# Optimization experiments

Measured on AMD Instinct MI355X. Metric: run time of the kernel, lower is better.

Reference implementation:

```python
import jax, jax.numpy as jnp
import numpy as np

D_MODEL = 1024
N_HEADS = 16
SEQ = 512  # == max_seq_len; rel-pos bias requires n_token == max_seq_len


def setup_inputs() -> dict:
    key = jax.random.key(0)
    ks = jax.random.split(key, 12)
    B = 16
    x = jax.random.normal(ks[0], (B, SEQ, D_MODEL), dtype=jnp.float32)
    c = jax.random.normal(ks[1], (B, SEQ, 8), dtype=jnp.float32)  # unused by forward
    s = 1.0 / np.sqrt(D_MODEL)
    Wq = jax.random.normal(ks[2], (D_MODEL, D_MODEL), dtype=jnp.float32) * s
    bq = jnp.zeros((D_MODEL,), dtype=jnp.float32)
    Wk = jax.random.normal(ks[3], (D_MODEL, D_MODEL), dtype=jnp.float32) * s
    bk = jnp.zeros((D_MODEL,), dtype=jnp.float32)
    Wv = jax.random.normal(ks[4], (D_MODEL, D_MODEL), dtype=jnp.float32) * s
    bv = jnp.zeros((D_MODEL,), dtype=jnp.float32)
    Wo = jax.random.normal(ks[5], (D_MODEL, D_MODEL), dtype=jnp.float32) * s
    bo = jnp.zeros((D_MODEL,), dtype=jnp.float32)
    # trunc_normal_(std=0.02) approximated by normal*0.02 (values stay small)
    rel_table = jax.random.normal(ks[6], (2 * SEQ - 1, N_HEADS), dtype=jnp.float32) * 0.02
    return {"x": x, "c": c, "Wq": Wq, "bq": bq, "Wk": Wk, "bk": bk,
            "Wv": Wv, "bv": bv, "Wo": Wo, "bo": bo, "rel_table": rel_table}


def reference(x, c, Wq, bq, Wk, bk, Wv, bv, Wo, bo, rel_table):
    # x: [B, S, D]; c is unused in the original forward
    B, S, D = x.shape
    H = N_HEADS
    dk = D // H
    scale = 1.0 / np.sqrt(dk)

    q = (x @ Wq + bq).reshape(B, S, H, dk)
    k = (x @ Wk + bk).reshape(B, S, H, dk)
    v = (x @ Wv + bv).reshape(B, S, H, dk)

    # scores: [B, H, S, S]
    scores = jnp.einsum('bihd,bjhd->bhij', q, k) * scale

    # relative position bias: index[i,j] = i + (S-1-j), values in [0, 2S-2]
    rel_index = jnp.arange(S)[:, None] + jnp.arange(S - 1, -1, -1)[None, :]  # [S,S]
    bias = rel_table[rel_index]            # [S, S, H]
    scores = scores + jnp.transpose(bias, (2, 0, 1))[None]  # [1,H,S,S]

    # causal_mask=False: original adds False * -1e9 == 0, so no mask term
    probs = jax.nn.softmax(scores, axis=-1)

    out = jnp.einsum('bhij,bjhd->bihd', probs, v).reshape(B, S, D)
    return out @ Wo + bo
```

## Files before the change

kernel.cpp:

```cpp
#include <hip/hip_runtime.h>
#include <hip/hip_bf16.h>
#include <stdint.h>

#define D_MODEL 1024
#define NH 16
#define SEQ 512
#define DK 64
#define BATCH 16
#define M_TOT (BATCH*SEQ)

typedef unsigned short u16;
typedef unsigned int u32;
typedef __attribute__((ext_vector_type(8))) __bf16 bf16x8;
typedef __attribute__((ext_vector_type(4))) u16 ushort4v;
typedef __attribute__((ext_vector_type(4))) float f32x4;

static __device__ __forceinline__ u16 f2bf(float f) {
    union { float f; u32 i; } c; c.f = f;
    return (u16)((c.i + 0x8000u) >> 16);
}
static __device__ __forceinline__ void async_copy16(const void* g, void* l) {
    __builtin_amdgcn_global_load_lds(
        (const __attribute__((address_space(1))) u32*)g,
        (__attribute__((address_space(3))) u32*)l, 16, 0, 0);
}

__global__ __launch_bounds__(256) void convert_f32_bf16(const float* __restrict__ in,
                                                        u16* __restrict__ out) {
    const int i = (blockIdx.x * 256 + threadIdx.x) * 4;
    float4 v = *(const float4*)&in[i];
    ushort4v o;
    o[0] = f2bf(v.x); o[1] = f2bf(v.y); o[2] = f2bf(v.z); o[3] = f2bf(v.w);
    *(ushort4v*)&out[i] = o;
}

__global__ __launch_bounds__(256) void transpose_w3(const float* __restrict__ W0,
                                                    const float* __restrict__ W1,
                                                    const float* __restrict__ W2,
                                                    u16* __restrict__ Wt) {
    __shared__ u16 tile[64][65];
    const int z = blockIdx.z;
    const float* W = (z == 0) ? W0 : (z == 1) ? W1 : W2;
    const int n0 = blockIdx.x * 64, k0 = blockIdx.y * 64;
    const int t = threadIdx.x;
    #pragma unroll
    for (int p = 0; p < 16; ++p) {
        int idx = p * 256 + t;
        int r = idx >> 6, c = idx & 63;
        tile[r][c] = f2bf(W[(size_t)(k0 + r) * D_MODEL + (n0 + c)]);
    }
    __syncthreads();
    #pragma unroll
    for (int p = 0; p < 16; ++p) {
        int idx = p * 256 + t;
        int r = idx >> 6, c = idx & 63;
        Wt[((size_t)z * D_MODEL + n0 + r) * D_MODEL + (k0 + c)] = tile[c][r];
    }
}

__global__ __launch_bounds__(256) void gemm_bt(const u16* __restrict__ A,
                                               const u16* __restrict__ Bt,
                                               const float* __restrict__ b0,
                                               const float* __restrict__ b1,
                                               const float* __restrict__ b2,
                                               void* __restrict__ o0,
                                               void* __restrict__ o1,
                                               void* __restrict__ o2,
                                               int qkv, int nb) {
    __shared__ __attribute__((aligned(16))) u16 smem[16896];
    u16* Asm = smem;
    u16* Bsm = smem + 8192;
    const int t = threadIdx.x;
    const int m0 = blockIdx.y * 128, n0 = (blockIdx.x + nb) * 128;
    const int lane = t & 63, w = t >> 6;
    const int lm = lane & 15, quad = lane >> 4;
    const int wm = w >> 1, wn = w & 1;

    f32x4 acc[4][4];
    #pragma unroll
    for (int i = 0; i < 4; ++i)
        #pragma unroll
        for (int j = 0; j < 4; ++j) acc[i][j] = (f32x4){0.f, 0.f, 0.f, 0.f};

    for (int kt = 0; kt < D_MODEL / 64; ++kt) {
        const int k0 = kt * 64;
        __syncthreads();
        #pragma unroll
        for (int i = 0; i < 4; ++i) {
            int chunk = i * 256 + t;
            int row = chunk >> 3, c = chunk & 7;
            int cs = c ^ (row & 7);
            async_copy16(A + (size_t)(m0 + row) * D_MODEL + k0 + cs * 8, &Asm[chunk * 8]);
        }
        #pragma unroll
        for (int i = 0; i < 4; ++i) {
            int chunk = i * 256 + t;
            int row = chunk >> 3, c = chunk & 7;
            int cs = c ^ (row & 7);
            async_copy16(Bt + (size_t)(n0 + row) * D_MODEL + k0 + cs * 8, &Bsm[chunk * 8]);
        }
        __syncthreads();
        #pragma unroll
        for (int ks = 0; ks < 64; ks += 32) {
            const int cbase = ks >> 3;
            bf16x8 af[4], bfv[4];
            #pragma unroll
            for (int im = 0; im < 4; ++im) {
                const int row = wm * 64 + im * 16 + lm;
                const int c = (cbase + quad) ^ (row & 7);
                af[im] = *(const bf16x8*)&Asm[row * 64 + c * 8];
            }
            #pragma unroll
            for (int in = 0; in < 4; ++in) {
                const int row = wn * 64 + in * 16 + lm;
                const int c = (cbase + quad) ^ (row & 7);
                bfv[in] = *(const bf16x8*)&Bsm[row * 64 + c * 8];
            }
            #pragma unroll
            for (int im = 0; im < 4; ++im)
                #pragma unroll
                for (int in = 0; in < 4; ++in)
                    acc[im][in] = __builtin_amdgcn_mfma_f32_16x16x32_bf16(
                        af[im], bfv[in], acc[im][in], 0, 0, 0);
        }
    }

    __syncthreads();
    if (qkv) {
        const int sel = n0 >> 10;
        if (sel == 2) {
            #pragma unroll
            for (int in = 0; in < 4; ++in) {
                const int nn = (n0 & 1023) + wn * 64 + in * 16 + lm;
                const float bv = b2[nn];
                const int h = nn >> 6, d = nn & 63;
                #pragma unroll
                for (int im = 0; im < 4; ++im) {
                    const int mb = m0 + wm * 64 + im * 16 + quad * 4;
                    const int b = mb >> 9, s = mb & 511;
                    ushort4v pk;
                    #pragma unroll
                    for (int r = 0; r < 4; ++r) pk[r] = f2bf(acc[im][in][r] + bv);
                    *(ushort4v*)&((u16*)o2)[((size_t)(b * NH + h) * DK + d) * SEQ + s] = pk;
                }
            }
        } else {
            u16* dst = sel ? (u16*)o1 : (u16*)o0;
            const float* bb = sel ? b1 : b0;
            u16 (*Cs)[132] = (u16(*)[132])smem;
            #pragma unroll
            for (int in = 0; in < 4; ++in) {
                const int nl = wn * 64 + in * 16 + lm;
                const float bv = bb[(n0 & 1023) + nl];
                #pragma unroll
                for (int im = 0; im < 4; ++im)
                    #pragma unroll
                    for (int r = 0; r < 4; ++r)
                        Cs[wm * 64 + im * 16 + quad * 4 + r][nl] =
                            f2bf(acc[im][in][r] + bv);
            }
            __syncthreads();
            const int rr = t >> 1, hh = t & 1;
            const int m = m0 + rr;
            const int b = m >> 9, s = m & 511;
            const int h = ((n0 & 1023) >> 6) + hh;
            u16* dp = &dst[((size_t)(b * NH + h) * SEQ + s) * DK];
            #pragma unroll
            for (int c = 0; c < 8; ++c)
                *(uint4*)&dp[c * 8] = *(const uint4*)&Cs[rr][hh * 64 + c * 8];
        }
    } else {
        float (*Cs)[132] = (float(*)[132])smem;
        #pragma unroll
        for (int ph = 0; ph < 2; ++ph) {
            if (wm == ph) {
                #pragma unroll
                for (int in = 0; in < 4; ++in) {
                    const int nl = wn * 64 + in * 16 + lm;
                    const float bv = b0[n0 + nl];
                    #pragma unroll
                    for (int im = 0; im < 4; ++im)
                        #pragma unroll
                        for (int r = 0; r < 4; ++r)
                            Cs[im * 16 + quad * 4 + r][nl] = acc[im][in][r] + bv;
                }
            }
            __syncthreads();
            const int rr = t >> 2, qq = t & 3;
            float* dp = &((float*)o0)[(size_t)(m0 + ph * 64 + rr) * D_MODEL + n0 + qq * 32];
            #pragma unroll
            for (int c = 0; c < 8; ++c)
                *(uint4*)&dp[c * 4] = *(const uint4*)&Cs[rr][qq * 32 + c * 4];
            __syncthreads();
        }
    }
}

__global__ __launch_bounds__(256) void attn_flash(const u16* __restrict__ qg,
                                                  const u16* __restrict__ kg,
                                                  const u16* __restrict__ vTg,
                                                  const float* __restrict__ rel,
                                                  u16* __restrict__ aout) {
    __shared__ __attribute__((aligned(16))) u16 qt[128 * 64];
    __shared__ __attribute__((aligned(16))) u16 kt[2][64 * 64];
    __shared__ __attribute__((aligned(16))) u16 vt[2][64 * 64];
    __shared__ __attribute__((aligned(16))) u16 Pl[4][32][72];
    __shared__ float biasb[640];

    const int t = threadIdx.x;
    const int lane = t & 63, w = t >> 6;
    const int lm = lane & 15, quad = lane >> 4;
    const int F = blockIdx.x;
    const int xcd = F & 7, qti = (F >> 3) & 3, grp = F >> 5;
    const int p = grp * 8 + xcd;
    const int h = p & 15, b = p >> 4;
    const int q0 = qti * 128;
    const size_t bh = (size_t)(b * NH + h);
    const u16* qb = qg + bh * SEQ * DK;
    const u16* kb = kg + bh * SEQ * DK;
    const u16* vb = vTg + bh * DK * SEQ;

    #pragma unroll
    for (int i = 0; i < 4; ++i) {
        const int chunk = i * 256 + t, row = chunk >> 3, c = chunk & 7;
        const int cs = c ^ (row & 7);
        *(uint4*)&qt[chunk * 8] = *(const uint4*)&qb[(q0 + row) * DK + cs * 8];
    }
    for (int u = t; u < 639; u += 256) biasb[u] = rel[(q0 + u) * NH + h];

    #pragma unroll
    for (int i = 0; i < 2; ++i) {
        const int chunk = i * 256 + t, row = chunk >> 3, c = chunk & 7;
        const int cs = c ^ (row & 7);
        async_copy16(kb + row * DK + cs * 8, &kt[0][chunk * 8]);
        async_copy16(vb + row * SEQ + cs * 8, &vt[0][chunk * 8]);
    }

    float lsum[2] = {0.f, 0.f};
    f32x4 o[2][4];
    #pragma unroll
    for (int g = 0; g < 2; ++g)
        #pragma unroll
        for (int sd = 0; sd < 4; ++sd) o[g][sd] = (f32x4){0.f, 0.f, 0.f, 0.f};

    const float scale = 0.125f;

    for (int jt = 0; jt < 8; ++jt) {
        __syncthreads();
        const int cur = jt & 1, nxt = cur ^ 1;
        if (jt < 7) {
            const int j1 = (jt + 1) * 64;
            #pragma unroll
            for (int i = 0; i < 2; ++i) {
                const int chunk = i * 256 + t, row = chunk >> 3, c = chunk & 7;
                const int cs = c ^ (row & 7);
                async_copy16(kb + (j1 + row) * DK + cs * 8, &kt[nxt][chunk * 8]);
                async_copy16(vb + row * SEQ + j1 + cs * 8, &vt[nxt][chunk * 8]);
            }
        }
        const int j0 = jt * 64;

        bf16x8 aq[2][2];
        #pragma unroll
        for (int g = 0; g < 2; ++g) {
            const int ra = w * 32 + g * 16 + lm;
            aq[g][0] = *(const bf16x8*)&qt[ra * 64 + ((quad) ^ (ra & 7)) * 8];
            aq[g][1] = *(const bf16x8*)&qt[ra * 64 + ((4 + quad) ^ (ra & 7)) * 8];
        }
        #pragma unroll
        for (int js = 0; js < 4; ++js) {
            const int rb = js * 16 + lm;
            bf16x8 bk0 = *(const bf16x8*)&kt[cur][rb * 64 + ((quad) ^ (rb & 7)) * 8];
            bf16x8 bk1 = *(const bf16x8*)&kt[cur][rb * 64 + ((4 + quad) ^ (rb & 7)) * 8];
            #pragma unroll
            for (int g = 0; g < 2; ++g) {
                f32x4 c = (f32x4){0.f, 0.f, 0.f, 0.f};
                c = __builtin_amdgcn_mfma_f32_16x16x32_bf16(bk0, aq[g][0], c, 0, 0, 0);
                c = __builtin_amdgcn_mfma_f32_16x16x32_bf16(bk1, aq[g][1], c, 0, 0, 0);
                const int bb0 = w * 32 + g * 16 + lm + 511 - j0 - js * 16 - quad * 4;
                ushort4v pk;
                #pragma unroll
                for (int r = 0; r < 4; ++r) {
                    float e = __expf(c[r] * scale + biasb[bb0 - r]);
                    lsum[g] += e;
                    pk[r] = f2bf(e);
                }
                *(ushort4v*)&Pl[w][g * 16 + lm][js * 16 + quad * 4] = pk;
            }
        }

        bf16x8 ap[2][2];
        #pragma unroll
        for (int g = 0; g < 2; ++g) {
            ap[g][0] = *(const bf16x8*)&Pl[w][g * 16 + lm][quad * 8];
            ap[g][1] = *(const bf16x8*)&Pl[w][g * 16 + lm][32 + quad * 8];
        }
        #pragma unroll
        for (int sd = 0; sd < 4; ++sd) {
            const int rv = sd * 16 + lm;
            bf16x8 bv0 = *(const bf16x8*)&vt[cur][rv * 64 + ((quad) ^ (rv & 7)) * 8];
            bf16x8 bv1 = *(const bf16x8*)&vt[cur][rv * 64 + ((4 + quad) ^ (rv & 7)) * 8];
            #pragma unroll
            for (int g = 0; g < 2; ++g) {
                o[g][sd] = __builtin_amdgcn_mfma_f32_16x16x32_bf16(bv0, ap[g][0], o[g][sd], 0, 0, 0);
                o[g][sd] = __builtin_amdgcn_mfma_f32_16x16x32_bf16(bv1, ap[g][1], o[g][sd], 0, 0, 0);
            }
        }
    }

    #pragma unroll
    for (int g = 0; g < 2; ++g) {
        float s = lsum[g];
        s += __shfl_xor(s, 16, 64);
        s += __shfl_xor(s, 32, 64);
        const float rinv = 1.0f / s;
        #pragma unroll
        for (int sd = 0; sd < 4; ++sd) {
            ushort4v pk;
            #pragma unroll
            for (int r = 0; r < 4; ++r) pk[r] = f2bf(o[g][sd][r] * rinv);
            *(ushort4v*)&Pl[w][g * 16 + lm][sd * 16 + quad * 4] = pk;
        }
    }
    const int rowl = lane >> 1, ch = lane & 1;
    u16* dp = aout + (size_t)(b * SEQ + q0 + w * 32 + rowl) * D_MODEL + h * DK + ch * 32;
    #pragma unroll
    for (int c = 0; c < 4; ++c)
        *(uint4*)&dp[c * 8] = *(const uint4*)&Pl[w][rowl][ch * 32 + c * 8];
}

extern "C" void kernel_launch(void* const* d_in, const int* in_sizes, int n_in,
                              void* d_out, int out_size, void* d_ws, size_t ws_size,
                              hipStream_t stream) {
    const float* x   = (const float*)d_in[0];
    const float* Wq  = (const float*)d_in[2];
    const float* bq  = (const float*)d_in[3];
    const float* Wk  = (const float*)d_in[4];
    const float* bk  = (const float*)d_in[5];
    const float* Wv  = (const float*)d_in[6];
    const float* bv  = (const float*)d_in[7];
    const float* Wo  = (const float*)d_in[8];
    const float* bo  = (const float*)d_in[9];
    const float* rel = (const float*)d_in[10];
    float* out = (float*)d_out;

    u16* ws = (u16*)d_ws;
    const size_t WSZ = (size_t)D_MODEL * D_MODEL;
    const size_t TSZ = (size_t)M_TOT * D_MODEL;
    u16* Wt3 = ws;
    u16* xbf = Wt3 + 3 * WSZ;
    u16* qws = xbf + TSZ;
    u16* kws = qws + TSZ;
    u16* vws = kws + TSZ;
    u16* aws = xbf;

    dim3 tb(256);
    convert_f32_bf16<<<dim3(M_TOT * D_MODEL / 1024), tb, 0, stream>>>(x, xbf);
    transpose_w3<<<dim3(16, 16, 3), tb, 0, stream>>>(Wq, Wk, Wv, Wt3);
    gemm_bt<<<dim3(8, 64), tb, 0, stream>>>(xbf, Wt3, bq, bk, bv, qws, kws, vws, 1, 0);
    gemm_bt<<<dim3(8, 64), tb, 0, stream>>>(xbf, Wt3, bq, bk, bv, qws, kws, vws, 1, 8);
    gemm_bt<<<dim3(8, 64), tb, 0, stream>>>(xbf, Wt3, bq, bk, bv, qws, kws, vws, 1, 16);
    attn_flash<<<dim3(1024), tb, 0, stream>>>(qws, kws, vws, rel, aws);
    transpose_w3<<<dim3(16, 16, 1), tb, 0, stream>>>(Wo, Wo, Wo, Wt3);
    gemm_bt<<<dim3(8, 64), tb, 0, stream>>>(aws, Wt3, bo, nullptr, nullptr,
                                            (void*)out, nullptr, nullptr, 0, 0);
}
```

Before: 270.7 us.

## Merge launches, fold Wo transpose into attention, use exp2 with pre-shifted bias

Merges the x conversion and QKV weight transpose into a single prep kernel. The three QKV GEMM launches become one 24x64 grid, and the Wo transpose runs as extra blocks inside the attention launch. In attention, the bias is pre-scaled by log2(e) and stored in four shifted copies so each lane can read it as one aligned vector, exp is done with raw v_exp_f32, and Q fragments are loaded once outside the key loop. The aim is to cut launch and tail overhead and per-element exp/bias cost, in exchange for a larger LDS footprint and one extra sync.

```diff
diff --git a/kernel.cpp b/kernel.cpp
--- a/kernel.cpp
+++ b/kernel.cpp
@@ -24,25 +24,31 @@
         (const __attribute__((address_space(1))) u32*)g,
         (__attribute__((address_space(3))) u32*)l, 16, 0, 0);
 }
-
-__global__ __launch_bounds__(256) void convert_f32_bf16(const float* __restrict__ in,
-                                                        u16* __restrict__ out) {
-    const int i = (blockIdx.x * 256 + threadIdx.x) * 4;
-    float4 v = *(const float4*)&in[i];
-    ushort4v o;
-    o[0] = f2bf(v.x); o[1] = f2bf(v.y); o[2] = f2bf(v.z); o[3] = f2bf(v.w);
-    *(ushort4v*)&out[i] = o;
-}
-
-__global__ __launch_bounds__(256) void transpose_w3(const float* __restrict__ W0,
-                                                    const float* __restrict__ W1,
-                                                    const float* __restrict__ W2,
-                                                    u16* __restrict__ Wt) {
+static __device__ __forceinline__ float fexp2(float x) {
+    float r; asm("v_exp_f32 %0, %1" : "=v"(r) : "v"(x)); return r;
+}
+
+__global__ __launch_bounds__(256) void prep(const float* __restrict__ x,
+                                            u16* __restrict__ xbf,
+                                            const float* __restrict__ Wq,
+                                            const float* __restrict__ Wk,
+                                            const float* __restrict__ Wv,
+                                            u16* __restrict__ Wt3) {
     __shared__ u16 tile[64][65];
-    const int z = blockIdx.z;
-    const float* W = (z == 0) ? W0 : (z == 1) ? W1 : W2;
-    const int n0 = blockIdx.x * 64, k0 = blockIdx.y * 64;
+    const int bid = blockIdx.x;
     const int t = threadIdx.x;
+    if (bid < 8192) {
+        const int i = (bid * 256 + t) * 4;
+        float4 v = *(const float4*)&x[i];
+        ushort4v o;
+        o[0] = f2bf(v.x); o[1] = f2bf(v.y); o[2] = f2bf(v.z); o[3] = f2bf(v.w);
+        *(ushort4v*)&xbf[i] = o;
+        return;
+    }
+    const int tw = bid - 8192;
+    const int z = tw >> 8;
+    const float* W = (z == 0) ? Wq : (z == 1) ? Wk : Wv;
+    const int n0 = (tw & 15) * 64, k0 = ((tw >> 4) & 15) * 64;
     #pragma unroll
     for (int p = 0; p < 16; ++p) {
         int idx = p * 256 + t;
@@ -54,7 +60,7 @@
     for (int p = 0; p < 16; ++p) {
         int idx = p * 256 + t;
         int r = idx >> 6, c = idx & 63;
-        Wt[((size_t)z * D_MODEL + n0 + r) * D_MODEL + (k0 + c)] = tile[c][r];
+        Wt3[((size_t)z * D_MODEL + n0 + r) * D_MODEL + (k0 + c)] = tile[c][r];
     }
 }
 
@@ -66,12 +72,12 @@
                                                void* __restrict__ o0,
                                                void* __restrict__ o1,
                                                void* __restrict__ o2,
-                                               int qkv, int nb) {
+                                               int qkv) {
     __shared__ __attribute__((aligned(16))) u16 smem[16896];
     u16* Asm = smem;
     u16* Bsm = smem + 8192;
     const int t = threadIdx.x;
-    const int m0 = blockIdx.y * 128, n0 = (blockIdx.x + nb) * 128;
+    const int m0 = blockIdx.y * 128, n0 = blockIdx.x * 128;
     const int lane = t & 63, w = t >> 6;
     const int lm = lane & 15, quad = lane >> 4;
     const int wm = w >> 1, wn = w & 1;
@@ -200,17 +206,39 @@
                                                   const u16* __restrict__ kg,
                                                   const u16* __restrict__ vTg,
                                                   const float* __restrict__ rel,
-                                                  u16* __restrict__ aout) {
+                                                  u16* __restrict__ aout,
+                                                  const float* __restrict__ Wo,
+                                                  u16* __restrict__ WtO) {
     __shared__ __attribute__((aligned(16))) u16 qt[128 * 64];
     __shared__ __attribute__((aligned(16))) u16 kt[2][64 * 64];
     __shared__ __attribute__((aligned(16))) u16 vt[2][64 * 64];
     __shared__ __attribute__((aligned(16))) u16 Pl[4][32][72];
-    __shared__ float biasb[640];
+    __shared__ __attribute__((aligned(16))) float bcs[4][648];
 
     const int t = threadIdx.x;
+    const int F = blockIdx.x;
+    if (F >= 1024) {
+        u16 (*tile)[65] = (u16(*)[65])qt;
+        const int tw = F - 1024;
+        const int n0 = (tw & 15) * 64, k0 = (tw >> 4) * 64;
+        #pragma unroll
+        for (int p = 0; p < 16; ++p) {
+            int idx = p * 256 + t;
+            int r = idx >> 6, c = idx & 63;
+            tile[r][c] = f2bf(Wo[(size_t)(k0 + r) * D_MODEL + (n0 + c)]);
+        }
+        __syncthreads();
+        #pragma unroll
+        for (int p = 0; p < 16; ++p) {
+            int idx = p * 256 + t;
+            int r = idx >> 6, c = idx & 63;
+            WtO[(size_t)(n0 + r) * D_MODEL + (k0 + c)] = tile[c][r];
+        }
+        return;
+    }
+
     const int lane = t & 63, w = t >> 6;
     const int lm = lane & 15, quad = lane >> 4;
-    const int F = blockIdx.x;
     const int xcd = F & 7, qti = (F >> 3) & 3, grp = F >> 5;
     const int p = grp * 8 + xcd;
     const int h = p & 15, b = p >> 4;
@@ -221,14 +249,6 @@
     const u16* vb = vTg + bh * DK * SEQ;
 
     #pragma unroll
-    for (int i = 0; i < 4; ++i) {
-        const int chunk = i * 256 + t, row = chunk >> 3, c = chunk & 7;
-        const int cs = c ^ (row & 7);
-        *(uint4*)&qt[chunk * 8] = *(const uint4*)&qb[(q0 + row) * DK + cs * 8];
-    }
-    for (int u = t; u < 639; u += 256) biasb[u] = rel[(q0 + u) * NH + h];
-
-    #pragma unroll
     for (int i = 0; i < 2; ++i) {
         const int chunk = i * 256 + t, row = chunk >> 3, c = chunk & 7;
         const int cs = c ^ (row & 7);
@@ -236,6 +256,28 @@
         async_copy16(vb + row * SEQ + cs * 8, &vt[0][chunk * 8]);
     }
 
+    #pragma unroll
+    for (int i = 0; i < 4; ++i) {
+        const int chunk = i * 256 + t, row = chunk >> 3, c = chunk & 7;
+        const int cs = c ^ (row & 7);
+        *(uint4*)&qt[chunk * 8] = *(const uint4*)&qb[(q0 + row) * DK + cs * 8];
+    }
+    for (int u = t; u < 639; u += 256) {
+        const float bv = rel[(q0 + u) * NH + h] * 1.44269504f;
+        #pragma unroll
+        for (int c = 0; c < 4; ++c) bcs[c][u + 4 - c] = bv;
+    }
+
+    __syncthreads();
+
+    bf16x8 aq[2][2];
+    #pragma unroll
+    for (int g = 0; g < 2; ++g) {
+        const int ra = w * 32 + g * 16 + lm;
+        aq[g][0] = *(const bf16x8*)&qt[ra * 64 + ((quad) ^ (ra & 7)) * 8];
+        aq[g][1] = *(const bf16x8*)&qt[ra * 64 + ((4 + quad) ^ (ra & 7)) * 8];
+    }
+
     float lsum[2] = {0.f, 0.f};
     f32x4 o[2][4];
     #pragma unroll
@@ -243,10 +285,12 @@
         #pragma unroll
         for (int sd = 0; sd < 4; ++sd) o[g][sd] = (f32x4){0.f, 0.f, 0.f, 0.f};
 
-    const float scale = 0.125f;
+    const float scale2 = 0.125f * 1.44269504f;
+    const int cc = lm & 3;
+    const int abase = w * 32 + lm + 512 - quad * 4 - cc;
 
     for (int jt = 0; jt < 8; ++jt) {
-        __syncthreads();
+        if (jt) __syncthreads();
         const int cur = jt & 1, nxt = cur ^ 1;
         if (jt < 7) {
             const int j1 = (jt + 1) * 64;
@@ -260,13 +304,6 @@
         }
         const int j0 = jt * 64;
 
-        bf16x8 aq[2][2];
-        #pragma unroll
-        for (int g = 0; g < 2; ++g) {
-            const int ra = w * 32 + g * 16 + lm;
-            aq[g][0] = *(const bf16x8*)&qt[ra * 64 + ((quad) ^ (ra & 7)) * 8];
-            aq[g][1] = *(const bf16x8*)&qt[ra * 64 + ((4 + quad) ^ (ra & 7)) * 8];
-        }
         #pragma unroll
         for (int js = 0; js < 4; ++js) {
             const int rb = js * 16 + lm;
@@ -277,11 +314,11 @@
                 f32x4 c = (f32x4){0.f, 0.f, 0.f, 0.f};
                 c = __builtin_amdgcn_mfma_f32_16x16x32_bf16(bk0, aq[g][0], c, 0, 0, 0);
                 c = __builtin_amdgcn_mfma_f32_16x16x32_bf16(bk1, aq[g][1], c, 0, 0, 0);
-                const int bb0 = w * 32 + g * 16 + lm + 511 - j0 - js * 16 - quad * 4;
+                const f32x4 bc4 = *(const f32x4*)&bcs[cc][abase + g * 16 - j0 - js * 16];
                 ushort4v pk;
                 #pragma unroll
                 for (int r = 0; r < 4; ++r) {
-                    float e = __expf(c[r] * scale + biasb[bb0 - r]);
+                    float e = fexp2(c[r] * scale2 + bc4[3 - r]);
                     lsum[g] += e;
                     pk[r] = f2bf(e);
                 }
@@ -355,13 +392,9 @@
     u16* aws = xbf;
 
     dim3 tb(256);
-    convert_f32_bf16<<<dim3(M_TOT * D_MODEL / 1024), tb, 0, stream>>>(x, xbf);
-    transpose_w3<<<dim3(16, 16, 3), tb, 0, stream>>>(Wq, Wk, Wv, Wt3);
-    gemm_bt<<<dim3(8, 64), tb, 0, stream>>>(xbf, Wt3, bq, bk, bv, qws, kws, vws, 1, 0);
-    gemm_bt<<<dim3(8, 64), tb, 0, stream>>>(xbf, Wt3, bq, bk, bv, qws, kws, vws, 1, 8);
-    gemm_bt<<<dim3(8, 64), tb, 0, stream>>>(xbf, Wt3, bq, bk, bv, qws, kws, vws, 1, 16);
-    attn_flash<<<dim3(1024), tb, 0, stream>>>(qws, kws, vws, rel, aws);
-    transpose_w3<<<dim3(16, 16, 1), tb, 0, stream>>>(Wo, Wo, Wo, Wt3);
+    prep<<<dim3(8192 + 768), tb, 0, stream>>>(x, xbf, Wq, Wk, Wv, Wt3);
+    gemm_bt<<<dim3(24, 64), tb, 0, stream>>>(xbf, Wt3, bq, bk, bv, qws, kws, vws, 1);
+    attn_flash<<<dim3(1024 + 256), tb, 0, stream>>>(qws, kws, vws, rel, aws, Wo, Wt3);
     gemm_bt<<<dim3(8, 64), tb, 0, stream>>>(aws, Wt3, bo, nullptr, nullptr,
-                                            (void*)out, nullptr, nullptr, 0, 0);
-}
+                                            (void*)out, nullptr, nullptr, 0);
+}
```

Result: faster. 256.2 us (-5.3%).
